# Kernel optimization log

Measured on AMD Instinct MI355X. Metric: run time of the kernel, lower is better.

Reference implementation:

```python
import jax, jax.numpy as jnp
import numpy as np

N_NODES = 15135


def setup_inputs() -> dict:
    key = jax.random.key(0)
    ks = jax.random.split(key, 12)
    bs, N, F_in, H, L, Hfc, C, E = 8, N_NODES, 64, 128, 3, 512, 10, 242160
    s = lambda k, *sh: jax.random.normal(k, sh, dtype=jnp.float32) * 0.05
    return {
        "x": jax.random.normal(ks[0], (bs, N, F_in), dtype=jnp.float32),
        "edge_index": jax.random.randint(ks[1], (2, E), 0, N),
        "W1": s(ks[2], F_in, H), "b1": jnp.zeros((H,), jnp.float32),
        "W2": s(ks[3], H, H),   "b2": jnp.zeros((H,), jnp.float32),
        "W3": s(ks[4], H, H),   "b3": jnp.zeros((H,), jnp.float32),
        "Wfc": s(ks[5], L * H, 1), "bfc": jnp.zeros((1,), jnp.float32),
        "Wl1": s(ks[6], N, Hfc), "bl1": jnp.zeros((Hfc,), jnp.float32),
        "Wl2": s(ks[7], Hfc, C), "bl2": jnp.zeros((C,), jnp.float32),
    }


def _gcn_norm(edge_index, num_nodes):
    # add self loops, compute symmetric normalization (PyG GCNConv default)
    loop = jnp.arange(num_nodes, dtype=edge_index.dtype)
    src = jnp.concatenate([edge_index[0], loop])
    dst = jnp.concatenate([edge_index[1], loop])
    deg = jax.ops.segment_sum(jnp.ones_like(dst, dtype=jnp.float32), dst,
                              num_segments=num_nodes)
    dinv = jax.lax.rsqrt(deg)  # deg >= 1 due to self-loops
    norm = dinv[src] * dinv[dst]
    return src, dst, norm


def _gcn_conv(x, W, b, src, dst, norm):
    # x: [bs, N, Fin] -> [bs, N, Fout]
    xl = jnp.einsum("bnf,fh->bnh", x, W)
    msg = xl[:, src, :] * norm[None, :, None]  # [bs, E+N, Fout]
    out = jnp.zeros_like(xl).at[:, dst].add(msg)
    return out + b


def reference(x, edge_index, W1, b1, W2, b2, W3, b3, Wfc, bfc, Wl1, bl1, Wl2, bl2):
    bs, N, _ = x.shape
    src, dst, norm = _gcn_norm(edge_index, N)
    h1 = jax.nn.relu(_gcn_conv(x, W1, b1, src, dst, norm))
    h2 = jax.nn.relu(_gcn_conv(h1, W2, b2, src, dst, norm))
    h3 = jax.nn.relu(_gcn_conv(h2, W3, b3, src, dst, norm))
    # mode='cat': torch.stack(xs, -1).view(bs, N, -1) interleaves features
    hcat = jnp.stack([h1, h2, h3], axis=-1).reshape(bs, N, -1)  # [bs,N,H*L]
    g = (jnp.einsum("bnk,ko->bno", hcat, Wfc) + bfc).reshape(bs, N)
    # dropout layers are identity in eval mode
    z = jax.nn.relu(g @ Wl1 + bl1)
    logits = z @ Wl2 + bl2
    return jax.nn.log_softmax(logits, axis=-1)
```

## Files before the change

kernel.cpp:

```cpp
#include <hip/hip_runtime.h>
#include <hip/hip_bf16.h>

#define NN 15135
#define BS 8
#define FIN 64
#define HD 128
#define EE 242160
#define HFC 512
#define NCLS 10

#define M_ROWS (BS * NN)
#define M_PAD  121088
#define PADE   287616

#define NCH 237
#define NPLANES (NCH * 2)

typedef __attribute__((ext_vector_type(8))) short bf16x8;
typedef __attribute__((ext_vector_type(4))) float f32x4;

__device__ __forceinline__ unsigned short to_bf16(float f) {
    unsigned u = __float_as_uint(f);
    u = (u + 0x7fffu + ((u >> 16) & 1u)) >> 16;
    return (unsigned short)u;
}
__device__ __forceinline__ unsigned pack2_bf16(float lo, float hi) {
    unsigned a = __float_as_uint(lo);
    unsigned b = __float_as_uint(hi);
    a = (a + 0x7fffu + ((a >> 16) & 1u)) >> 16;
    b = (b + 0x7fffu + ((b >> 16) & 1u)) & 0xffff0000u;
    return (a & 0xffffu) | b;
}

__global__ void k_deg(const int* __restrict__ dst, int* __restrict__ degi) {
    int e = blockIdx.x * 256 + threadIdx.x;
    if (e < EE) atomicAdd(&degi[dst[e]], 1);
}

#define SCAN_T 1024
#define SCAN_PER 15
__global__ __launch_bounds__(SCAN_T) void k_scan(const int* __restrict__ degi,
                                                 int* __restrict__ row_ptr,
                                                 float* __restrict__ dinv) {
    __shared__ int part[SCAN_T];
    const int t = threadIdx.x;
    const int base = t * SCAN_PER;
    int loc[SCAN_PER];
    int s = 0;
#pragma unroll
    for (int i = 0; i < SCAN_PER; i++) {
        int d = (base + i < NN) ? degi[base + i] : 0;
        if (base + i < NN) dinv[base + i] = rsqrtf((float)d + 1.0f);
        int pd = (d + 3) & ~3;
        loc[i] = s; s += pd;
    }
    part[t] = s;
    __syncthreads();
    for (int off = 1; off < SCAN_T; off <<= 1) {
        int v = (t >= off) ? part[t - off] : 0;
        __syncthreads();
        part[t] += v;
        __syncthreads();
    }
    int before = (t == 0) ? 0 : part[t - 1];
#pragma unroll
    for (int i = 0; i < SCAN_PER; i++)
        if (base + i < NN) row_ptr[base + i] = before + loc[i];
    if (t == SCAN_T - 1) row_ptr[NN] = part[SCAN_T - 1];
}

__global__ void k_bucket(const int* __restrict__ src, const int* __restrict__ dst,
                         const int* __restrict__ row_ptr, int* __restrict__ cursor,
                         const float* __restrict__ dinv,
                         int* __restrict__ s_idx, float* __restrict__ wts) {
    int e = blockIdx.x * 256 + threadIdx.x;
    if (e >= EE) return;
    int s = src[e], d = dst[e];
    int pos = atomicAdd(&cursor[d], 1);
    int idx = row_ptr[d] + pos;
    s_idx[idx] = s;
    wts[idx] = dinv[s] * dinv[d];
}

__global__ void k_cvtW(const float* __restrict__ W1, const float* __restrict__ W2,
                       const float* __restrict__ W3, unsigned short* __restrict__ Wt) {
    int idx = blockIdx.x * 256 + threadIdx.x;
    const float* W; int K, base;
    if (idx < 8192)       { W = W1; K = 64;  base = idx; }
    else if (idx < 24576) { W = W2; K = 128; base = idx - 8192; }
    else                  { W = W3; K = 128; base = idx - 24576; }
    int c = base / K, k = base % K;
    Wt[idx] = to_bf16(W[(size_t)k * HD + c]);
}

__global__ __launch_bounds__(256) void k_aggx(const float* __restrict__ x,
                                              const int* __restrict__ row_ptr,
                                              const int* __restrict__ s_idx,
                                              const float* __restrict__ wts,
                                              const float* __restrict__ dinv,
                                              unsigned short* __restrict__ Ab) {
    const int tid = threadIdx.x;
    const int widx = tid >> 6, lane = tid & 63;
    const int n = blockIdx.x * 4 + widx;
    if (n >= NN) return;
    const int bb = blockIdx.y * 2 + (lane >> 5);
    const int fp = lane & 31;
    const float* Xs = x + (size_t)bb * NN * FIN + 2 * fp;

    const int e0 = __builtin_amdgcn_readfirstlane(row_ptr[n]);
    const int e1 = __builtin_amdgcn_readfirstlane(row_ptr[n + 1]);
    const float dv = dinv[n];

    float2 v = *(const float2*)&Xs[(size_t)n * FIN];
    float ax = dv * dv * v.x, ay = dv * dv * v.y;

    for (int c = e0; c < e1; c += 4) {
        int s0 = s_idx[c + 0], s1 = s_idx[c + 1], s2 = s_idx[c + 2], s3 = s_idx[c + 3];
        float w0 = wts[c + 0], w1 = wts[c + 1], w2 = wts[c + 2], w3 = wts[c + 3];
        float2 u0 = *(const float2*)&Xs[(size_t)s0 * FIN];
        float2 u1 = *(const float2*)&Xs[(size_t)s1 * FIN];
        float2 u2 = *(const float2*)&Xs[(size_t)s2 * FIN];
        float2 u3 = *(const float2*)&Xs[(size_t)s3 * FIN];
        ax += w0 * u0.x; ay += w0 * u0.y;
        ax += w1 * u1.x; ay += w1 * u1.y;
        ax += w2 * u2.x; ay += w2 * u2.y;
        ax += w3 * u3.x; ay += w3 * u3.y;
    }
    *(unsigned*)&Ab[(size_t)bb * NN * FIN + (size_t)n * FIN + 2 * fp] = pack2_bf16(ax, ay);
}

__global__ __launch_bounds__(256) void k_agg128(const unsigned short* __restrict__ Xb,
                                                const int* __restrict__ row_ptr,
                                                const int* __restrict__ s_idx,
                                                const float* __restrict__ wts,
                                                const float* __restrict__ dinv,
                                                unsigned short* __restrict__ Ab) {
    const int tid = threadIdx.x;
    const int widx = tid >> 6, lane = tid & 63;
    const int n = blockIdx.x * 4 + widx;
    if (n >= NN) return;
    const int bb = blockIdx.y;
    const int fp = lane;
    const unsigned short* Xs = Xb + (size_t)bb * NN * HD + 2 * fp;

    const int e0 = __builtin_amdgcn_readfirstlane(row_ptr[n]);
    const int e1 = __builtin_amdgcn_readfirstlane(row_ptr[n + 1]);
    const float dv = dinv[n];

    float ax, ay;
    {
        unsigned u = *(const unsigned*)&Xs[(size_t)n * HD];
        float w0 = dv * dv;
        ax = w0 * __uint_as_float(u << 16);
        ay = w0 * __uint_as_float(u & 0xffff0000u);
    }
    for (int c = e0; c < e1; c += 4) {
        int s0 = s_idx[c + 0], s1 = s_idx[c + 1], s2 = s_idx[c + 2], s3 = s_idx[c + 3];
        float w0 = wts[c + 0], w1 = wts[c + 1], w2 = wts[c + 2], w3 = wts[c + 3];
        unsigned u0 = *(const unsigned*)&Xs[(size_t)s0 * HD];
        unsigned u1 = *(const unsigned*)&Xs[(size_t)s1 * HD];
        unsigned u2 = *(const unsigned*)&Xs[(size_t)s2 * HD];
        unsigned u3 = *(const unsigned*)&Xs[(size_t)s3 * HD];
        ax += w0 * __uint_as_float(u0 << 16); ay += w0 * __uint_as_float(u0 & 0xffff0000u);
        ax += w1 * __uint_as_float(u1 << 16); ay += w1 * __uint_as_float(u1 & 0xffff0000u);
        ax += w2 * __uint_as_float(u2 << 16); ay += w2 * __uint_as_float(u2 & 0xffff0000u);
        ax += w3 * __uint_as_float(u3 << 16); ay += w3 * __uint_as_float(u3 & 0xffff0000u);
    }
    *(unsigned*)&Ab[(size_t)bb * NN * HD + (size_t)n * HD + 2 * fp] = pack2_bf16(ax, ay);
}

template<int KD, int LIDX, bool GINIT, bool STOREH>
__global__ __launch_bounds__(256) void k_gemm_ep(const unsigned short* __restrict__ Xb,
                                                 const unsigned short* __restrict__ Wt,
                                                 const float* __restrict__ bias,
                                                 const float* __restrict__ Wfc,
                                                 const float* __restrict__ bfc,
                                                 unsigned short* __restrict__ H,
                                                 float* __restrict__ g) {
    constexpr int NK = KD / 32;
    const int tid = threadIdx.x;
    const int w = tid >> 6, lane = tid & 63;
    const int l15 = lane & 15, lhi = lane >> 4;
    const int row0 = blockIdx.x * 64;
    const int cbase = w * 32;

    bf16x8 B[2][NK];
#pragma unroll
    for (int ct = 0; ct < 2; ct++)
#pragma unroll
        for (int ks = 0; ks < NK; ks++)
            B[ct][ks] = *(const bf16x8*)&Wt[(size_t)(cbase + ct * 16 + l15) * KD + ks * 32 + lhi * 8];

    f32x4 acc[4][2] = {};
#pragma unroll
    for (int ks = 0; ks < NK; ks++) {
        bf16x8 A[4];
#pragma unroll
        for (int rt = 0; rt < 4; rt++)
            A[rt] = *(const bf16x8*)&Xb[(size_t)(row0 + rt * 16 + l15) * KD + ks * 32 + lhi * 8];
#pragma unroll
        for (int rt = 0; rt < 4; rt++)
#pragma unroll
            for (int ct = 0; ct < 2; ct++)
                acc[rt][ct] = __builtin_amdgcn_mfma_f32_16x16x32_bf16(A[rt], B[ct][ks], acc[rt][ct], 0, 0, 0);
    }

    __shared__ float gred[4][64];
    const float bias0 = bias[cbase + l15], bias1 = bias[cbase + 16 + l15];
    const float wf0 = Wfc[(cbase + l15) * 3 + LIDX];
    const float wf1 = Wfc[(cbase + 16 + l15) * 3 + LIDX];
#pragma unroll
    for (int rt = 0; rt < 4; rt++) {
#pragma unroll
        for (int reg = 0; reg < 4; reg++) {
            const int row = row0 + rt * 16 + lhi * 4 + reg;
            float h0 = fmaxf(acc[rt][0][reg] + bias0, 0.f);
            float h1 = fmaxf(acc[rt][1][reg] + bias1, 0.f);
            if (STOREH) {
                H[(size_t)row * 128 + cbase + l15] = to_bf16(h0);
                H[(size_t)row * 128 + cbase + 16 + l15] = to_bf16(h1);
            }
            float p = h0 * wf0 + h1 * wf1;
#pragma unroll
            for (int m = 8; m; m >>= 1) p += __shfl_xor(p, m, 64);
            if (l15 == 0) gred[w][rt * 16 + lhi * 4 + reg] = p;
        }
    }
    __syncthreads();
    if (tid < 64) {
        const int row = row0 + tid;
        if (row < M_ROWS) {
            float s = gred[0][tid] + gred[1][tid] + gred[2][tid] + gred[3][tid];
            if (GINIT) g[row] = bfc[0] + s; else g[row] += s;
        }
    }
}

__global__ __launch_bounds__(256) void k_fc1part(const float* __restrict__ g,
                                                 const float* __restrict__ Wl1,
                                                 float* __restrict__ part) {
    const int ct = threadIdx.x & 127;
    const int st = threadIdx.x >> 7;
    const int n0 = blockIdx.x * 64;
    __shared__ float gs[BS][64];
    for (int i = threadIdx.x; i < BS * 64; i += 256) {
        int b = i >> 6, j = i & 63;
        int n = n0 + j;
        gs[b][j] = (n < NN) ? g[b * NN + n] : 0.f;
    }
    __syncthreads();

    f32x4 acc[BS] = {};
    const int jend = min(64, NN - n0);
#pragma unroll 4
    for (int j = st; j < jend; j += 2) {
        f32x4 wv = *(const f32x4*)&Wl1[(size_t)(n0 + j) * HFC + 4 * ct];
#pragma unroll
        for (int b = 0; b < BS; b++) {
            float gv = gs[b][j];
            acc[b] += gv * wv;
        }
    }
    float* p = &part[((size_t)(blockIdx.x * 2 + st)) * (BS * HFC)];
#pragma unroll
    for (int b = 0; b < BS; b++)
        *(f32x4*)&p[b * HFC + 4 * ct] = acc[b];
}

__global__ __launch_bounds__(128) void k_fc1red(const float* __restrict__ part,
                                                const float* __restrict__ bl1,
                                                float* __restrict__ z) {
    const int idx = blockIdx.x * 128 + threadIdx.x;
    float s = 0.f;
#pragma unroll 8
    for (int y = 0; y < NPLANES; y++) s += part[(size_t)y * (BS * HFC) + idx];
    const int c = idx & 511;
    z[idx] = fmaxf(s + bl1[c], 0.f);
}

__global__ void k_head(const float* __restrict__ z, const float* __restrict__ Wl2,
                       const float* __restrict__ bl2, float* __restrict__ out) {
    __shared__ float lg[BS][NCLS];
    const int t = threadIdx.x;
    if (t < BS * NCLS) {
        int b = t / NCLS, c = t % NCLS;
        float a = bl2[c];
        for (int k = 0; k < HFC; k++) a += z[b * HFC + k] * Wl2[k * NCLS + c];
        lg[b][c] = a;
    }
    __syncthreads();
    if (t < BS * NCLS) {
        int b = t / NCLS, c = t % NCLS;
        float m = -1e30f;
#pragma unroll
        for (int j = 0; j < NCLS; j++) m = fmaxf(m, lg[b][j]);
        float s = 0.f;
#pragma unroll
        for (int j = 0; j < NCLS; j++) s += expf(lg[b][j] - m);
        out[b * NCLS + c] = lg[b][c] - m - logf(s);
    }
}

extern "C" void kernel_launch(void* const* d_in, const int* in_sizes, int n_in,
                              void* d_out, int out_size, void* d_ws, size_t ws_size,
                              hipStream_t stream) {
    const float* x   = (const float*)d_in[0];
    const int*   ei  = (const int*)d_in[1];
    const float* W1  = (const float*)d_in[2];
    const float* b1  = (const float*)d_in[3];
    const float* W2  = (const float*)d_in[4];
    const float* b2  = (const float*)d_in[5];
    const float* W3  = (const float*)d_in[6];
    const float* b3  = (const float*)d_in[7];
    const float* Wfc = (const float*)d_in[8];
    const float* bfc = (const float*)d_in[9];
    const float* Wl1 = (const float*)d_in[10];
    const float* bl1 = (const float*)d_in[11];
    const float* Wl2 = (const float*)d_in[12];
    const float* bl2 = (const float*)d_in[13];
    float* out = (float*)d_out;

    const int* srcp = ei;
    const int* dstp = ei + EE;

    float* ws = (float*)d_ws;
    float* dinv    = ws;
    float* g       = ws + 15360;
    float* z       = ws + 136448;
    float* part    = ws + 140544;
    int*   degi    = (int*)(ws + 2082048);
    int*   cursor  = (int*)(ws + 2097408);
    int*   row_ptr = (int*)(ws + 2112768);
    int*   s_idx   = (int*)(ws + 2128256);
    float* wts     = ws + 2415872;
    unsigned short* Wt  = (unsigned short*)(ws + 2703488);
    unsigned short* Wt1 = Wt;
    unsigned short* Wt2 = Wt + 8192;
    unsigned short* Wt3 = Wt + 24576;
    unsigned short* a0  = (unsigned short*)(ws + 2723968);
    unsigned short* B1  = (unsigned short*)(ws + 6598784);
    unsigned short* B2  = (unsigned short*)(ws + 14348416);

    const int gemm_grid = M_PAD / 64;

    hipMemsetAsync(degi, 0, 2 * 15360 * sizeof(int), stream);
    hipMemsetAsync(s_idx, 0, 2 * PADE * sizeof(int), stream);
    k_deg<<<(EE + 255) / 256, 256, 0, stream>>>(dstp, degi);
    k_scan<<<1, SCAN_T, 0, stream>>>(degi, row_ptr, dinv);
    k_bucket<<<(EE + 255) / 256, 256, 0, stream>>>(srcp, dstp, row_ptr, cursor, dinv, s_idx, wts);
    k_cvtW<<<160, 256, 0, stream>>>(W1, W2, W3, Wt);

    k_aggx<<<dim3((NN + 3) / 4, 4), 256, 0, stream>>>(x, row_ptr, s_idx, wts, dinv, a0);
    k_gemm_ep<64, 0, true, true><<<gemm_grid, 256, 0, stream>>>(a0, Wt1, b1, Wfc, bfc, B1, g);
    k_agg128<<<dim3((NN + 3) / 4, 8), 256, 0, stream>>>(B1, row_ptr, s_idx, wts, dinv, B2);
    k_gemm_ep<128, 1, false, true><<<gemm_grid, 256, 0, stream>>>(B2, Wt2, b2, Wfc, bfc, B1, g);
    k_agg128<<<dim3((NN + 3) / 4, 8), 256, 0, stream>>>(B1, row_ptr, s_idx, wts, dinv, B2);
    k_gemm_ep<128, 2, false, false><<<gemm_grid, 256, 0, stream>>>(B2, Wt3, b3, Wfc, bfc, B1, g);

    k_fc1part<<<NCH, 256, 0, stream>>>(g, Wl1, part);
    k_fc1red<<<32, 128, 0, stream>>>(part, bl1, z);
    k_head<<<1, 128, 0, stream>>>(z, Wl2, bl2, out);
}
```

Baseline: 491.9 us.

## Fuse GCN aggregation with MFMA GEMM epilogue per 64-node tile

Each GCN layer's sparse aggregation and its dense bf16 MFMA GEMM plus bias/ReLU/Wfc epilogue now run in one kernel per 64-node tile and batch. The aggregated tile goes into swizzled LDS instead of a global intermediate buffer. CSR index and weight arrays are interleaved into int2 pairs and staged through LDS in chunks. This removes three launches and the global write and read of aggregated activations. In exchange each wave carries 16 per-node accumulators, which adds register pressure, and the per-node edge loops are serialized within a wave.

```diff
diff --git a/kernel.cpp b/kernel.cpp
--- a/kernel.cpp
+++ b/kernel.cpp
@@ -10,8 +10,9 @@
 #define NCLS 10
 
 #define M_ROWS (BS * NN)
-#define M_PAD  121088
 #define PADE   287616
+#define NT     237
+#define CAP    2048
 
 #define NCH 237
 #define NPLANES (NCH * 2)
@@ -71,15 +72,12 @@
 
 __global__ void k_bucket(const int* __restrict__ src, const int* __restrict__ dst,
                          const int* __restrict__ row_ptr, int* __restrict__ cursor,
-                         const float* __restrict__ dinv,
-                         int* __restrict__ s_idx, float* __restrict__ wts) {
+                         const float* __restrict__ dinv, int2* __restrict__ csr) {
     int e = blockIdx.x * 256 + threadIdx.x;
     if (e >= EE) return;
     int s = src[e], d = dst[e];
     int pos = atomicAdd(&cursor[d], 1);
-    int idx = row_ptr[d] + pos;
-    s_idx[idx] = s;
-    wts[idx] = dinv[s] * dinv[d];
+    csr[row_ptr[d] + pos] = make_int2(s, __float_as_int(dinv[s] * dinv[d]));
 }
 
 __global__ void k_cvtW(const float* __restrict__ W1, const float* __restrict__ W2,
@@ -93,111 +91,222 @@
     Wt[idx] = to_bf16(W[(size_t)k * HD + c]);
 }
 
-__global__ __launch_bounds__(256) void k_aggx(const float* __restrict__ x,
-                                              const int* __restrict__ row_ptr,
-                                              const int* __restrict__ s_idx,
-                                              const float* __restrict__ wts,
-                                              const float* __restrict__ dinv,
-                                              unsigned short* __restrict__ Ab) {
+__global__ __launch_bounds__(256) void k_conv1(const float* __restrict__ x,
+                                               const int2* __restrict__ csr,
+                                               const int* __restrict__ rp,
+                                               const float* __restrict__ dinv,
+                                               const unsigned short* __restrict__ Wt,
+                                               const float* __restrict__ bias,
+                                               const float* __restrict__ Wfc,
+                                               const float* __restrict__ bfc,
+                                               unsigned short* __restrict__ H,
+                                               float* __restrict__ g) {
+    __shared__ int4 smem[CAP / 2];
+    __shared__ float gred[4][64];
     const int tid = threadIdx.x;
     const int widx = tid >> 6, lane = tid & 63;
-    const int n = blockIdx.x * 4 + widx;
-    if (n >= NN) return;
-    const int bb = blockIdx.y * 2 + (lane >> 5);
-    const int fp = lane & 31;
-    const float* Xs = x + (size_t)bb * NN * FIN + 2 * fp;
-
-    const int e0 = __builtin_amdgcn_readfirstlane(row_ptr[n]);
-    const int e1 = __builtin_amdgcn_readfirstlane(row_ptr[n + 1]);
-    const float dv = dinv[n];
-
-    float2 v = *(const float2*)&Xs[(size_t)n * FIN];
-    float ax = dv * dv * v.x, ay = dv * dv * v.y;
-
-    for (int c = e0; c < e1; c += 4) {
-        int s0 = s_idx[c + 0], s1 = s_idx[c + 1], s2 = s_idx[c + 2], s3 = s_idx[c + 3];
-        float w0 = wts[c + 0], w1 = wts[c + 1], w2 = wts[c + 2], w3 = wts[c + 3];
-        float2 u0 = *(const float2*)&Xs[(size_t)s0 * FIN];
-        float2 u1 = *(const float2*)&Xs[(size_t)s1 * FIN];
-        float2 u2 = *(const float2*)&Xs[(size_t)s2 * FIN];
-        float2 u3 = *(const float2*)&Xs[(size_t)s3 * FIN];
-        ax += w0 * u0.x; ay += w0 * u0.y;
-        ax += w1 * u1.x; ay += w1 * u1.y;
-        ax += w2 * u2.x; ay += w2 * u2.y;
-        ax += w3 * u3.x; ay += w3 * u3.y;
-    }
-    *(unsigned*)&Ab[(size_t)bb * NN * FIN + (size_t)n * FIN + 2 * fp] = pack2_bf16(ax, ay);
-}
-
-__global__ __launch_bounds__(256) void k_agg128(const unsigned short* __restrict__ Xb,
-                                                const int* __restrict__ row_ptr,
-                                                const int* __restrict__ s_idx,
-                                                const float* __restrict__ wts,
+    const int bb = blockIdx.y;
+    const int t0 = blockIdx.x * 64;
+    const float* Xbase = x + (size_t)bb * NN * FIN;
+
+    int rpi = t0 + widx * 16 + (lane <= 16 ? lane : 16);
+    int rpv = rp[rpi < NN ? rpi : NN];
+    int e0[16], e1[16];
+    float ax[16];
+#pragma unroll
+    for (int i = 0; i < 16; i++) {
+        e0[i] = __shfl(rpv, i, 64);
+        e1[i] = __shfl(rpv, i + 1, 64);
+        int n = t0 + widx * 16 + i;
+        if (n < NN) {
+            float dv = dinv[n];
+            ax[i] = dv * dv * Xbase[(size_t)n * FIN + lane];
+        } else ax[i] = 0.f;
+    }
+    const int blockBase = __builtin_amdgcn_readfirstlane(rp[t0]);
+    const int tEnd = (t0 + 64 < NN) ? t0 + 64 : NN;
+    const int blockEnd = __builtin_amdgcn_readfirstlane(rp[tEnd]);
+
+    for (int cb = blockBase; cb < blockEnd; cb += CAP) {
+        const int ce = (cb + CAP < blockEnd) ? cb + CAP : blockEnd;
+        const int np4 = (ce - cb) >> 1;
+        const int4* gsrc = (const int4*)(csr + cb);
+        for (int j = tid; j < np4; j += 256) smem[j] = gsrc[j];
+        __syncthreads();
+#pragma unroll
+        for (int i = 0; i < 16; i++) {
+            int a = e0[i] > cb ? e0[i] : cb;
+            int b = e1[i] < ce ? e1[i] : ce;
+            for (int e = a; e < b; e += 4) {
+                int4 m0 = smem[(e - cb) >> 1];
+                int4 m1 = smem[((e - cb) >> 1) + 1];
+                float u0 = Xbase[(size_t)m0.x * FIN + lane];
+                float u1 = Xbase[(size_t)m0.z * FIN + lane];
+                float u2 = Xbase[(size_t)m1.x * FIN + lane];
+                float u3 = Xbase[(size_t)m1.z * FIN + lane];
+                ax[i] += __int_as_float(m0.y) * u0;
+                ax[i] += __int_as_float(m0.w) * u1;
+                ax[i] += __int_as_float(m1.y) * u2;
+                ax[i] += __int_as_float(m1.w) * u3;
+            }
+        }
+        __syncthreads();
+    }
+    unsigned short* As = (unsigned short*)smem;
+#pragma unroll
+    for (int i = 0; i < 16; i++) {
+        int r = widx * 16 + i;
+        int byte = (r * 128 + lane * 2) ^ ((r & 7) << 4);
+        *(unsigned short*)((char*)As + byte) = to_bf16(ax[i]);
+    }
+    __syncthreads();
+
+    const int l15 = lane & 15, lhi = lane >> 4;
+    const int cbase = widx * 32;
+    bf16x8 B[2][2];
+#pragma unroll
+    for (int ct = 0; ct < 2; ct++)
+#pragma unroll
+        for (int ks = 0; ks < 2; ks++)
+            B[ct][ks] = *(const bf16x8*)&Wt[(size_t)(cbase + ct * 16 + l15) * 64 + ks * 32 + lhi * 8];
+    f32x4 acc[4][2] = {};
+#pragma unroll
+    for (int ks = 0; ks < 2; ks++) {
+        bf16x8 A[4];
+#pragma unroll
+        for (int rt = 0; rt < 4; rt++) {
+            int r = rt * 16 + l15;
+            int byte = (r * 128 + ks * 64 + lhi * 16) ^ ((r & 7) << 4);
+            A[rt] = *(const bf16x8*)((const char*)As + byte);
+        }
+#pragma unroll
+        for (int rt = 0; rt < 4; rt++)
+#pragma unroll
+            for (int ct = 0; ct < 2; ct++)
+                acc[rt][ct] = __builtin_amdgcn_mfma_f32_16x16x32_bf16(A[rt], B[ct][ks], acc[rt][ct], 0, 0, 0);
+    }
+
+    const float bias0 = bias[cbase + l15], bias1 = bias[cbase + 16 + l15];
+    const float wf0 = Wfc[(cbase + l15) * 3 + 0];
+    const float wf1 = Wfc[(cbase + 16 + l15) * 3 + 0];
+#pragma unroll
+    for (int rt = 0; rt < 4; rt++) {
+#pragma unroll
+        for (int reg = 0; reg < 4; reg++) {
+            const int lr = rt * 16 + lhi * 4 + reg;
+            const int n = t0 + lr;
+            float h0 = fmaxf(acc[rt][0][reg] + bias0, 0.f);
+            float h1 = fmaxf(acc[rt][1][reg] + bias1, 0.f);
+            if (n < NN) {
+                H[((size_t)bb * NN + n) * HD + cbase + l15] = to_bf16(h0);
+                H[((size_t)bb * NN + n) * HD + cbase + 16 + l15] = to_bf16(h1);
+            }
+            float p = h0 * wf0 + h1 * wf1;
+#pragma unroll
+            for (int m = 8; m; m >>= 1) p += __shfl_xor(p, m, 64);
+            if (l15 == 0) gred[widx][lr] = p;
+        }
+    }
+    __syncthreads();
+    if (tid < 64) {
+        const int n = t0 + tid;
+        if (n < NN) g[bb * NN + n] = bfc[0] + gred[0][tid] + gred[1][tid] + gred[2][tid] + gred[3][tid];
+    }
+}
+
+template<int LIDX, bool STOREH>
+__global__ __launch_bounds__(256) void k_conv23(const unsigned short* __restrict__ Xb,
+                                                const int2* __restrict__ csr,
+                                                const int* __restrict__ rp,
                                                 const float* __restrict__ dinv,
-                                                unsigned short* __restrict__ Ab) {
+                                                const unsigned short* __restrict__ Wt,
+                                                const float* __restrict__ bias,
+                                                const float* __restrict__ Wfc,
+                                                unsigned short* __restrict__ H,
+                                                float* __restrict__ g) {
+    __shared__ int4 smem[CAP / 2];
+    __shared__ float gred[4][64];
     const int tid = threadIdx.x;
     const int widx = tid >> 6, lane = tid & 63;
-    const int n = blockIdx.x * 4 + widx;
-    if (n >= NN) return;
     const int bb = blockIdx.y;
-    const int fp = lane;
-    const unsigned short* Xs = Xb + (size_t)bb * NN * HD + 2 * fp;
-
-    const int e0 = __builtin_amdgcn_readfirstlane(row_ptr[n]);
-    const int e1 = __builtin_amdgcn_readfirstlane(row_ptr[n + 1]);
-    const float dv = dinv[n];
-
-    float ax, ay;
-    {
-        unsigned u = *(const unsigned*)&Xs[(size_t)n * HD];
-        float w0 = dv * dv;
-        ax = w0 * __uint_as_float(u << 16);
-        ay = w0 * __uint_as_float(u & 0xffff0000u);
-    }
-    for (int c = e0; c < e1; c += 4) {
-        int s0 = s_idx[c + 0], s1 = s_idx[c + 1], s2 = s_idx[c + 2], s3 = s_idx[c + 3];
-        float w0 = wts[c + 0], w1 = wts[c + 1], w2 = wts[c + 2], w3 = wts[c + 3];
-        unsigned u0 = *(const unsigned*)&Xs[(size_t)s0 * HD];
-        unsigned u1 = *(const unsigned*)&Xs[(size_t)s1 * HD];
-        unsigned u2 = *(const unsigned*)&Xs[(size_t)s2 * HD];
-        unsigned u3 = *(const unsigned*)&Xs[(size_t)s3 * HD];
-        ax += w0 * __uint_as_float(u0 << 16); ay += w0 * __uint_as_float(u0 & 0xffff0000u);
-        ax += w1 * __uint_as_float(u1 << 16); ay += w1 * __uint_as_float(u1 & 0xffff0000u);
-        ax += w2 * __uint_as_float(u2 << 16); ay += w2 * __uint_as_float(u2 & 0xffff0000u);
-        ax += w3 * __uint_as_float(u3 << 16); ay += w3 * __uint_as_float(u3 & 0xffff0000u);
-    }
-    *(unsigned*)&Ab[(size_t)bb * NN * HD + (size_t)n * HD + 2 * fp] = pack2_bf16(ax, ay);
-}
-
-template<int KD, int LIDX, bool GINIT, bool STOREH>
-__global__ __launch_bounds__(256) void k_gemm_ep(const unsigned short* __restrict__ Xb,
-                                                 const unsigned short* __restrict__ Wt,
-                                                 const float* __restrict__ bias,
-                                                 const float* __restrict__ Wfc,
-                                                 const float* __restrict__ bfc,
-                                                 unsigned short* __restrict__ H,
-                                                 float* __restrict__ g) {
-    constexpr int NK = KD / 32;
-    const int tid = threadIdx.x;
-    const int w = tid >> 6, lane = tid & 63;
+    const int t0 = blockIdx.x * 64;
+    const unsigned short* Xbase = Xb + (size_t)bb * NN * HD;
+
+    int rpi = t0 + widx * 16 + (lane <= 16 ? lane : 16);
+    int rpv = rp[rpi < NN ? rpi : NN];
+    int e0[16], e1[16];
+    float ax[16], ay[16];
+#pragma unroll
+    for (int i = 0; i < 16; i++) {
+        e0[i] = __shfl(rpv, i, 64);
+        e1[i] = __shfl(rpv, i + 1, 64);
+        int n = t0 + widx * 16 + i;
+        if (n < NN) {
+            float dv = dinv[n];
+            float w0 = dv * dv;
+            unsigned u = *(const unsigned*)&Xbase[(size_t)n * HD + lane * 2];
+            ax[i] = w0 * __uint_as_float(u << 16);
+            ay[i] = w0 * __uint_as_float(u & 0xffff0000u);
+        } else { ax[i] = 0.f; ay[i] = 0.f; }
+    }
+    const int blockBase = __builtin_amdgcn_readfirstlane(rp[t0]);
+    const int tEnd = (t0 + 64 < NN) ? t0 + 64 : NN;
+    const int blockEnd = __builtin_amdgcn_readfirstlane(rp[tEnd]);
+
+    for (int cb = blockBase; cb < blockEnd; cb += CAP) {
+        const int ce = (cb + CAP < blockEnd) ? cb + CAP : blockEnd;
+        const int np4 = (ce - cb) >> 1;
+        const int4* gsrc = (const int4*)(csr + cb);
+        for (int j = tid; j < np4; j += 256) smem[j] = gsrc[j];
+        __syncthreads();
+#pragma unroll
+        for (int i = 0; i < 16; i++) {
+            int a = e0[i] > cb ? e0[i] : cb;
+            int b = e1[i] < ce ? e1[i] : ce;
+            for (int e = a; e < b; e += 4) {
+                int4 m0 = smem[(e - cb) >> 1];
+                int4 m1 = smem[((e - cb) >> 1) + 1];
+                unsigned u0 = *(const unsigned*)&Xbase[(size_t)m0.x * HD + lane * 2];
+                unsigned u1 = *(const unsigned*)&Xbase[(size_t)m0.z * HD + lane * 2];
+                unsigned u2 = *(const unsigned*)&Xbase[(size_t)m1.x * HD + lane * 2];
+                unsigned u3 = *(const unsigned*)&Xbase[(size_t)m1.z * HD + lane * 2];
+                float w0 = __int_as_float(m0.y), w1 = __int_as_float(m0.w);
+                float w2 = __int_as_float(m1.y), w3 = __int_as_float(m1.w);
+                ax[i] += w0 * __uint_as_float(u0 << 16); ay[i] += w0 * __uint_as_float(u0 & 0xffff0000u);
+                ax[i] += w1 * __uint_as_float(u1 << 16); ay[i] += w1 * __uint_as_float(u1 & 0xffff0000u);
+                ax[i] += w2 * __uint_as_float(u2 << 16); ay[i] += w2 * __uint_as_float(u2 & 0xffff0000u);
+                ax[i] += w3 * __uint_as_float(u3 << 16); ay[i] += w3 * __uint_as_float(u3 & 0xffff0000u);
+            }
+        }
+        __syncthreads();
+    }
+    unsigned short* As = (unsigned short*)smem;
+#pragma unroll
+    for (int i = 0; i < 16; i++) {
+        int r = widx * 16 + i;
+        int byte = (r * 256 + lane * 4) ^ ((r & 7) << 4);
+        *(unsigned*)((char*)As + byte) = pack2_bf16(ax[i], ay[i]);
+    }
+    __syncthreads();
+
     const int l15 = lane & 15, lhi = lane >> 4;
-    const int row0 = blockIdx.x * 64;
-    const int cbase = w * 32;
-
-    bf16x8 B[2][NK];
+    const int cbase = widx * 32;
+    bf16x8 B[2][4];
 #pragma unroll
     for (int ct = 0; ct < 2; ct++)
 #pragma unroll
-        for (int ks = 0; ks < NK; ks++)
-            B[ct][ks] = *(const bf16x8*)&Wt[(size_t)(cbase + ct * 16 + l15) * KD + ks * 32 + lhi * 8];
-
+        for (int ks = 0; ks < 4; ks++)
+            B[ct][ks] = *(const bf16x8*)&Wt[(size_t)(cbase + ct * 16 + l15) * HD + ks * 32 + lhi * 8];
     f32x4 acc[4][2] = {};
 #pragma unroll
-    for (int ks = 0; ks < NK; ks++) {
+    for (int ks = 0; ks < 4; ks++) {
         bf16x8 A[4];
 #pragma unroll
-        for (int rt = 0; rt < 4; rt++)
-            A[rt] = *(const bf16x8*)&Xb[(size_t)(row0 + rt * 16 + l15) * KD + ks * 32 + lhi * 8];
+        for (int rt = 0; rt < 4; rt++) {
+            int r = rt * 16 + l15;
+            int byte = (r * 256 + ks * 64 + lhi * 16) ^ ((r & 7) << 4);
+            A[rt] = *(const bf16x8*)((const char*)As + byte);
+        }
 #pragma unroll
         for (int rt = 0; rt < 4; rt++)
 #pragma unroll
@@ -205,7 +314,6 @@
                 acc[rt][ct] = __builtin_amdgcn_mfma_f32_16x16x32_bf16(A[rt], B[ct][ks], acc[rt][ct], 0, 0, 0);
     }
 
-    __shared__ float gred[4][64];
     const float bias0 = bias[cbase + l15], bias1 = bias[cbase + 16 + l15];
     const float wf0 = Wfc[(cbase + l15) * 3 + LIDX];
     const float wf1 = Wfc[(cbase + 16 + l15) * 3 + LIDX];
@@ -213,26 +321,24 @@
     for (int rt = 0; rt < 4; rt++) {
 #pragma unroll
         for (int reg = 0; reg < 4; reg++) {
-            const int row = row0 + rt * 16 + lhi * 4 + reg;
+            const int lr = rt * 16 + lhi * 4 + reg;
+            const int n = t0 + lr;
             float h0 = fmaxf(acc[rt][0][reg] + bias0, 0.f);
             float h1 = fmaxf(acc[rt][1][reg] + bias1, 0.f);
-            if (STOREH) {
-                H[(size_t)row * 128 + cbase + l15] = to_bf16(h0);
-                H[(size_t)row * 128 + cbase + 16 + l15] = to_bf16(h1);
+            if (STOREH && n < NN) {
+                H[((size_t)bb * NN + n) * HD + cbase + l15] = to_bf16(h0);
+                H[((size_t)bb * NN + n) * HD + cbase + 16 + l15] = to_bf16(h1);
             }
             float p = h0 * wf0 + h1 * wf1;
 #pragma unroll
             for (int m = 8; m; m >>= 1) p += __shfl_xor(p, m, 64);
-            if (l15 == 0) gred[w][rt * 16 + lhi * 4 + reg] = p;
+            if (l15 == 0) gred[widx][lr] = p;
         }
     }
     __syncthreads();
     if (tid < 64) {
-        const int row = row0 + tid;
-        if (row < M_ROWS) {
-            float s = gred[0][tid] + gred[1][tid] + gred[2][tid] + gred[3][tid];
-            if (GINIT) g[row] = bfc[0] + s; else g[row] += s;
-        }
+        const int n = t0 + tid;
+        if (n < NN) g[bb * NN + n] += gred[0][tid] + gred[1][tid] + gred[2][tid] + gred[3][tid];
     }
 }
 
@@ -251,15 +357,12 @@
     __syncthreads();
 
     f32x4 acc[BS] = {};
-    const int jend = min(64, NN - n0);
+    const int jend = (64 < NN - n0) ? 64 : NN - n0;
 #pragma unroll 4
     for (int j = st; j < jend; j += 2) {
         f32x4 wv = *(const f32x4*)&Wl1[(size_t)(n0 + j) * HFC + 4 * ct];
 #pragma unroll
-        for (int b = 0; b < BS; b++) {
-            float gv = gs[b][j];
-            acc[b] += gv * wv;
-        }
+        for (int b = 0; b < BS; b++) acc[b] += gs[b][j] * wv;
     }
     float* p = &part[((size_t)(blockIdx.x * 2 + st)) * (BS * HFC)];
 #pragma unroll
@@ -274,8 +377,7 @@
     float s = 0.f;
 #pragma unroll 8
     for (int y = 0; y < NPLANES; y++) s += part[(size_t)y * (BS * HFC) + idx];
-    const int c = idx & 511;
-    z[idx] = fmaxf(s + bl1[c], 0.f);
+    z[idx] = fmaxf(s + bl1[idx & 511], 0.f);
 }
 
 __global__ void k_head(const float* __restrict__ z, const float* __restrict__ Wl2,
@@ -331,31 +433,24 @@
     int*   degi    = (int*)(ws + 2082048);
     int*   cursor  = (int*)(ws + 2097408);
     int*   row_ptr = (int*)(ws + 2112768);
-    int*   s_idx   = (int*)(ws + 2128256);
-    float* wts     = ws + 2415872;
+    int2*  csr     = (int2*)(ws + 2128256);
     unsigned short* Wt  = (unsigned short*)(ws + 2703488);
     unsigned short* Wt1 = Wt;
     unsigned short* Wt2 = Wt + 8192;
     unsigned short* Wt3 = Wt + 24576;
-    unsigned short* a0  = (unsigned short*)(ws + 2723968);
-    unsigned short* B1  = (unsigned short*)(ws + 6598784);
-    unsigned short* B2  = (unsigned short*)(ws + 14348416);
-
-    const int gemm_grid = M_PAD / 64;
+    unsigned short* B1  = (unsigned short*)(ws + 2723968);
+    unsigned short* B2  = (unsigned short*)(ws + 10473600);
 
     hipMemsetAsync(degi, 0, 2 * 15360 * sizeof(int), stream);
-    hipMemsetAsync(s_idx, 0, 2 * PADE * sizeof(int), stream);
+    hipMemsetAsync(csr, 0, (size_t)PADE * 8, stream);
     k_deg<<<(EE + 255) / 256, 256, 0, stream>>>(dstp, degi);
     k_scan<<<1, SCAN_T, 0, stream>>>(degi, row_ptr, dinv);
-    k_bucket<<<(EE + 255) / 256, 256, 0, stream>>>(srcp, dstp, row_ptr, cursor, dinv, s_idx, wts);
+    k_bucket<<<(EE + 255) / 256, 256, 0, stream>>>(srcp, dstp, row_ptr, cursor, dinv, csr);
     k_cvtW<<<160, 256, 0, stream>>>(W1, W2, W3, Wt);
 
-    k_aggx<<<dim3((NN + 3) / 4, 4), 256, 0, stream>>>(x, row_ptr, s_idx, wts, dinv, a0);
-    k_gemm_ep<64, 0, true, true><<<gemm_grid, 256, 0, stream>>>(a0, Wt1, b1, Wfc, bfc, B1, g);
-    k_agg128<<<dim3((NN + 3) / 4, 8), 256, 0, stream>>>(B1, row_ptr, s_idx, wts, dinv, B2);
-    k_gemm_ep<128, 1, false, true><<<gemm_grid, 256, 0, stream>>>(B2, Wt2, b2, Wfc, bfc, B1, g);
-    k_agg128<<<dim3((NN + 3) / 4, 8), 256, 0, stream>>>(B1, row_ptr, s_idx, wts, dinv, B2);
-    k_gemm_ep<128, 2, false, false><<<gemm_grid, 256, 0, stream>>>(B2, Wt3, b3, Wfc, bfc, B1, g);
+    k_conv1<<<dim3(NT, 8), 256, 0, stream>>>(x, csr, row_ptr, dinv, Wt1, b1, Wfc, bfc, B1, g);
+    k_conv23<1, true><<<dim3(NT, 8), 256, 0, stream>>>(B1, csr, row_ptr, dinv, Wt2, b2, Wfc, B2, g);
+    k_conv23<2, false><<<dim3(NT, 8), 256, 0, stream>>>(B2, csr, row_ptr, dinv, Wt3, b3, Wfc, nullptr, g);
 
     k_fc1part<<<NCH, 256, 0, stream>>>(g, Wl1, part);
     k_fc1red<<<32, 128, 0, stream>>>(part, bl1, z);
```

Result: slower. 639.2 us (+30.0%).
